# Kernel optimization log

Measured on AMD Instinct MI355X. Metric: run time of the kernel, lower is better.

## Reference

```python
import jax, jax.numpy as jnp
import numpy as np

B, S, H, A = 64, 4096, 256, 128


def entmax15(z):
    # exact entmax-1.5 along the last axis (Peters & Martins 2019)
    z = z / 2.0
    z = z - jnp.max(z, axis=-1, keepdims=True)
    zs = -jnp.sort(-z, axis=-1)                      # descending sort
    n = zs.shape[-1]
    k = jnp.arange(1, n + 1, dtype=z.dtype)
    mean = jnp.cumsum(zs, axis=-1) / k
    mean_sq = jnp.cumsum(zs * zs, axis=-1) / k
    ss = k * (mean_sq - mean * mean)
    delta = jnp.clip((1.0 - ss) / k, 0.0)
    tau = mean - jnp.sqrt(delta)
    k_star = jnp.sum(tau <= zs, axis=-1)             # support size per row
    tau_star = jnp.take_along_axis(tau, (k_star - 1)[..., None], axis=-1)
    return jnp.square(jnp.clip(z - tau_star, 0.0))


def setup_inputs() -> dict:
    key = jax.random.key(0)
    k0, k1, k2, k3, k4 = jax.random.split(key, 5)
    lim1 = 1.0 / np.sqrt(H)
    lim2 = 1.0 / np.sqrt(A)
    return {
        "lstm_output": jax.random.normal(k0, (B, S, H), dtype=jnp.float32),
        "W1": jax.random.uniform(k1, (H, A), jnp.float32, -lim1, lim1),
        "b1": jax.random.uniform(k2, (A,), jnp.float32, -lim1, lim1),
        "W2": jax.random.uniform(k3, (A, 1), jnp.float32, -lim2, lim2),
        "b2": jax.random.uniform(k4, (1,), jnp.float32, -lim2, lim2),
    }


def reference(lstm_output, W1, b1, W2, b2):
    # score MLP: Linear -> Tanh -> Linear -> squeeze(-1)  => [B, S]
    h = jnp.tanh(jnp.einsum("bsh,ha->bsa", lstm_output, W1) + b1)
    scores = (jnp.einsum("bsa,ao->bso", h, W2) + b2)[..., 0]
    weights = entmax15(scores)                       # entmax over seq axis (dim=1)
    context = jnp.einsum("bsh,bs->bh", lstm_output, weights)
    return (context, weights)
```

## Files before the change

### kernel.cpp

```cpp
#include <hip/hip_runtime.h>
#include <hip/hip_bf16.h>

#define BB 64
#define SS 4096
#define HH 256
#define AA 128
#define MT 128
#define WST 264

typedef __fp16 fp16v2 __attribute__((ext_vector_type(2)));
typedef _Float16 half8v __attribute__((ext_vector_type(8)));
typedef float floatx16 __attribute__((ext_vector_type(16)));

__device__ __forceinline__ float fast_tanh(float x) {
    float xc = fminf(fmaxf(x, -9.0f), 9.0f);
    float e = __expf(2.0f * xc);
    return 1.0f - __fdividef(2.0f, e + 1.0f);
}

__global__ void convert_w1(const float* __restrict__ W1, _Float16* __restrict__ Wt) {
    int n = blockIdx.x;
    int k = threadIdx.x;
    Wt[n * HH + k] = (_Float16)W1[k * AA + n];
}

__global__ __launch_bounds__(256, 2) void score_mfma(
    const float* __restrict__ X,
    const _Float16* __restrict__ Wt,
    const float* __restrict__ b1,
    const float* __restrict__ W2,
    const float* __restrict__ b2,
    float* __restrict__ scores)
{
    __shared__ _Float16 Ws2[128 * WST];

    const int tid   = threadIdx.x;
    const int m0    = blockIdx.x * MT;
    const int wid   = tid >> 6;
    const int lane  = tid & 63;
    const int lrow  = lane & 31;
    const int lhalf = lane >> 5;

    #pragma unroll
    for (int p = 0; p < 16; ++p) {
        int idx = tid + p * 256;
        int row = idx >> 5, u = idx & 31;
        *(uint4*)(Ws2 + row * WST + u * 8) =
            *(const uint4*)(Wt + (size_t)row * HH + u * 8);
    }
    __syncthreads();

    floatx16 acc[4];
    #pragma unroll
    for (int nb = 0; nb < 4; ++nb)
        #pragma unroll
        for (int r = 0; r < 16; ++r) acc[nb][r] = 0.0f;

    const float* xrow = X + (size_t)(m0 + wid * 32 + lrow) * HH + lhalf * 8;

    float4 a0 = *(const float4*)(xrow);
    float4 a1 = *(const float4*)(xrow + 4);
    #pragma unroll
    for (int s = 0; s < 16; ++s) {
        float4 n0 = a0, n1 = a1;
        if (s < 15) {
            n0 = *(const float4*)(xrow + (s + 1) * 16);
            n1 = *(const float4*)(xrow + (s + 1) * 16 + 4);
        }
        union { fp16v2 h2[4]; half8v h8; } ua;
        ua.h2[0] = __builtin_amdgcn_cvt_pkrtz(a0.x, a0.y);
        ua.h2[1] = __builtin_amdgcn_cvt_pkrtz(a0.z, a0.w);
        ua.h2[2] = __builtin_amdgcn_cvt_pkrtz(a1.x, a1.y);
        ua.h2[3] = __builtin_amdgcn_cvt_pkrtz(a1.z, a1.w);
        #pragma unroll
        for (int nb = 0; nb < 4; ++nb) {
            half8v bf = *(half8v*)(Ws2 + (nb * 32 + lrow) * WST + s * 16 + lhalf * 8);
            acc[nb] = __builtin_amdgcn_mfma_f32_32x32x16_f16(ua.h8, bf, acc[nb], 0, 0, 0);
        }
        a0 = n0; a1 = n1;
    }

    const float b2v = b2[0];
    float b1v[4], w2v[4];
    #pragma unroll
    for (int nb = 0; nb < 4; ++nb) {
        b1v[nb] = b1[nb * 32 + lrow];
        w2v[nb] = W2[nb * 32 + lrow];
    }
    #pragma unroll
    for (int r = 0; r < 16; ++r) {
        float s = 0.0f;
        #pragma unroll
        for (int nb = 0; nb < 4; ++nb)
            s += fast_tanh(acc[nb][r] + b1v[nb]) * w2v[nb];
        #pragma unroll
        for (int o = 1; o < 32; o <<= 1) s += __shfl_xor(s, o);
        if (lrow == 0) {
            int ridx = (r & 3) + 8 * (r >> 2) + 4 * lhalf;
            scores[m0 + wid * 32 + ridx] = s + b2v;
        }
    }
}

__global__ __launch_bounds__(256) void entmax_ctx_kernel(
    const float* __restrict__ X, float* __restrict__ buf, float* __restrict__ ctx)
{
    __shared__ float sred[8];
    __shared__ int   cnt;
    __shared__ int   sidx[SS];
    __shared__ float swt[SS];

    const int b = blockIdx.x, tid = threadIdx.x;
    const int wid = tid >> 6;
    float* p = buf + (size_t)b * SS;
    const float4* p4 = (const float4*)p;

    if (tid == 0) cnt = 0;

    float z[16];
    #pragma unroll
    for (int jj = 0; jj < 4; ++jj) {
        float4 v = p4[tid * 4 + jj];
        z[jj * 4 + 0] = v.x * 0.5f; z[jj * 4 + 1] = v.y * 0.5f;
        z[jj * 4 + 2] = v.z * 0.5f; z[jj * 4 + 3] = v.w * 0.5f;
    }

    float m = -1e30f;
    #pragma unroll
    for (int j = 0; j < 16; ++j) m = fmaxf(m, z[j]);
    #pragma unroll
    for (int o = 1; o < 64; o <<= 1) m = fmaxf(m, __shfl_xor(m, o));
    if ((tid & 63) == 0) sred[wid] = m;
    __syncthreads();
    m = fmaxf(fmaxf(sred[0], sred[1]), fmaxf(sred[2], sred[3]));
    __syncthreads();
    #pragma unroll
    for (int j = 0; j < 16; ++j) z[j] -= m;

    float lo = -1.0f, hi = 0.0f;
    #pragma unroll 1
    for (int it = 0; it < 10; ++it) {
        float tau = 0.5f * (lo + hi);
        float s0 = 0.f, s1 = 0.f, s2 = 0.f, s3 = 0.f;
        #pragma unroll
        for (int j = 0; j < 16; j += 4) {
            float d0 = fmaxf(z[j]     - tau, 0.0f);
            float d1 = fmaxf(z[j + 1] - tau, 0.0f);
            float d2 = fmaxf(z[j + 2] - tau, 0.0f);
            float d3 = fmaxf(z[j + 3] - tau, 0.0f);
            s0 = fmaf(d0, d0, s0); s1 = fmaf(d1, d1, s1);
            s2 = fmaf(d2, d2, s2); s3 = fmaf(d3, d3, s3);
        }
        float s = (s0 + s1) + (s2 + s3);
        #pragma unroll
        for (int o = 1; o < 64; o <<= 1) s += __shfl_xor(s, o);
        if ((tid & 63) == 0) sred[wid] = s;
        __syncthreads();
        s = (sred[0] + sred[1]) + (sred[2] + sred[3]);
        __syncthreads();
        if (s >= 1.0f) lo = tau; else hi = tau;
    }

    float tau = lo;
    #pragma unroll 1
    for (int it = 0; it < 4; ++it) {
        float s0 = 0.f, s1 = 0.f, t0 = 0.f, t1 = 0.f;
        #pragma unroll
        for (int j = 0; j < 16; j += 2) {
            float d0 = fmaxf(z[j]     - tau, 0.0f);
            float d1 = fmaxf(z[j + 1] - tau, 0.0f);
            s0 = fmaf(d0, d0, s0); s1 = fmaf(d1, d1, s1);
            t0 += d0; t1 += d1;
        }
        float s = s0 + s1, t = t0 + t1;
        #pragma unroll
        for (int o = 1; o < 64; o <<= 1) {
            s += __shfl_xor(s, o);
            t += __shfl_xor(t, o);
        }
        if ((tid & 63) == 0) { sred[wid * 2] = s; sred[wid * 2 + 1] = t; }
        __syncthreads();
        s = (sred[0] + sred[2]) + (sred[4] + sred[6]);
        t = (sred[1] + sred[3]) + (sred[5] + sred[7]);
        __syncthreads();
        tau = fminf(tau + (s - 1.0f) / (2.0f * t + 1e-30f), hi);
    }

    float4* p4w = (float4*)p;
    #pragma unroll
    for (int jj = 0; jj < 4; ++jj) {
        float w[4];
        #pragma unroll
        for (int k = 0; k < 4; ++k) {
            float d = fmaxf(z[jj * 4 + k] - tau, 0.0f);
            w[k] = d * d;
            if (w[k] > 0.0f) {
                int pos = atomicAdd(&cnt, 1);
                sidx[pos] = tid * 16 + jj * 4 + k;
                swt[pos]  = w[k];
            }
        }
        p4w[tid * 4 + jj] = make_float4(w[0], w[1], w[2], w[3]);
    }
    __syncthreads();

    const int n = cnt;
    const float* xb = X + (size_t)b * SS * HH + tid;
    float a0 = 0.f, a1 = 0.f, a2 = 0.f, a3 = 0.f;
    int i = 0;
    for (; i + 4 <= n; i += 4) {
        a0 = fmaf(swt[i    ], xb[(size_t)sidx[i    ] * HH], a0);
        a1 = fmaf(swt[i + 1], xb[(size_t)sidx[i + 1] * HH], a1);
        a2 = fmaf(swt[i + 2], xb[(size_t)sidx[i + 2] * HH], a2);
        a3 = fmaf(swt[i + 3], xb[(size_t)sidx[i + 3] * HH], a3);
    }
    for (; i < n; ++i) a0 = fmaf(swt[i], xb[(size_t)sidx[i] * HH], a0);
    ctx[b * HH + tid] = (a0 + a1) + (a2 + a3);
}

extern "C" void kernel_launch(void* const* d_in, const int* in_sizes, int n_in,
                              void* d_out, int out_size, void* d_ws, size_t ws_size,
                              hipStream_t stream) {
    const float* X  = (const float*)d_in[0];
    const float* W1 = (const float*)d_in[1];
    const float* b1 = (const float*)d_in[2];
    const float* W2 = (const float*)d_in[3];
    const float* b2 = (const float*)d_in[4];

    float* out = (float*)d_out;
    float* ctx = out;
    float* wts = out + BB * HH;
    _Float16* Wt = (_Float16*)d_ws;

    convert_w1<<<AA, HH, 0, stream>>>(W1, Wt);
    score_mfma<<<(BB * SS) / MT, 256, 0, stream>>>(X, Wt, b1, W2, b2, wts);
    entmax_ctx_kernel<<<BB, 256, 0, stream>>>(X, wts, ctx);
}
```

Before: 406.7 us.

## Stage X and W1 tiles through LDS with direct global-to-LDS loads

The score kernel now loops over K in chunks of 64. Each chunk loads both the fp32 X tile and the fp16 W1 tile into XOR-swizzled shared memory using global_load_lds, where before X was read per lane directly from global memory and all of W1 was preloaded. This gives coalesced X loads and cuts LDS per block, so occupancy goes up (launch bounds 3). In exchange it adds two barriers per chunk and gives up the register prefetch overlap between loads and MFMA.

```diff
diff --git a/kernel.cpp b/kernel.cpp
--- a/kernel.cpp
+++ b/kernel.cpp
@@ -6,7 +6,7 @@
 #define HH 256
 #define AA 128
 #define MT 128
-#define WST 264
+#define BK 64
 
 typedef __fp16 fp16v2 __attribute__((ext_vector_type(2)));
 typedef _Float16 half8v __attribute__((ext_vector_type(8)));
@@ -24,7 +24,7 @@
     Wt[n * HH + k] = (_Float16)W1[k * AA + n];
 }
 
-__global__ __launch_bounds__(256, 2) void score_mfma(
+__global__ __launch_bounds__(256, 3) void score_mfma(
     const float* __restrict__ X,
     const _Float16* __restrict__ Wt,
     const float* __restrict__ b1,
@@ -32,7 +32,9 @@
     const float* __restrict__ b2,
     float* __restrict__ scores)
 {
-    __shared__ _Float16 Ws2[128 * WST];
+    __shared__ __align__(16) char smem[49152];
+    float*    Xs = (float*)smem;
+    _Float16* Ws = (_Float16*)(smem + 32768);
 
     const int tid   = threadIdx.x;
     const int m0    = blockIdx.x * MT;
@@ -41,43 +43,59 @@
     const int lrow  = lane & 31;
     const int lhalf = lane >> 5;
 
-    #pragma unroll
-    for (int p = 0; p < 16; ++p) {
-        int idx = tid + p * 256;
-        int row = idx >> 5, u = idx & 31;
-        *(uint4*)(Ws2 + row * WST + u * 8) =
-            *(const uint4*)(Wt + (size_t)row * HH + u * 8);
-    }
-    __syncthreads();
-
     floatx16 acc[4];
     #pragma unroll
     for (int nb = 0; nb < 4; ++nb)
         #pragma unroll
         for (int r = 0; r < 16; ++r) acc[nb][r] = 0.0f;
 
-    const float* xrow = X + (size_t)(m0 + wid * 32 + lrow) * HH + lhalf * 8;
-
-    float4 a0 = *(const float4*)(xrow);
-    float4 a1 = *(const float4*)(xrow + 4);
-    #pragma unroll
-    for (int s = 0; s < 16; ++s) {
-        float4 n0 = a0, n1 = a1;
-        if (s < 15) {
-            n0 = *(const float4*)(xrow + (s + 1) * 16);
-            n1 = *(const float4*)(xrow + (s + 1) * 16 + 4);
-        }
-        union { fp16v2 h2[4]; half8v h8; } ua;
-        ua.h2[0] = __builtin_amdgcn_cvt_pkrtz(a0.x, a0.y);
-        ua.h2[1] = __builtin_amdgcn_cvt_pkrtz(a0.z, a0.w);
-        ua.h2[2] = __builtin_amdgcn_cvt_pkrtz(a1.x, a1.y);
-        ua.h2[3] = __builtin_amdgcn_cvt_pkrtz(a1.z, a1.w);
-        #pragma unroll
-        for (int nb = 0; nb < 4; ++nb) {
-            half8v bf = *(half8v*)(Ws2 + (nb * 32 + lrow) * WST + s * 16 + lhalf * 8);
-            acc[nb] = __builtin_amdgcn_mfma_f32_32x32x16_f16(ua.h8, bf, acc[nb], 0, 0, 0);
-        }
-        a0 = n0; a1 = n1;
+    const int rl  = wid * 32 + lrow;
+    const int swz = rl & 7;
+
+    for (int k0 = 0; k0 < HH; k0 += BK) {
+        #pragma unroll
+        for (int p = 0; p < 8; ++p) {
+            int S = (p * 4 + wid) * 64 + lane;
+            int r = S >> 4;
+            int c = (S & 15) ^ (r & 7);
+            const float* gp = X + (size_t)(m0 + r) * HH + k0 + c * 4;
+            __builtin_amdgcn_global_load_lds(
+                (const __attribute__((address_space(1))) void*)gp,
+                (__attribute__((address_space(3))) void*)(smem + (p * 4 + wid) * 1024),
+                16, 0, 0);
+        }
+        #pragma unroll
+        for (int p = 0; p < 4; ++p) {
+            int S = (p * 4 + wid) * 64 + lane;
+            int r = S >> 3;
+            int c = (S & 7) ^ (r & 7);
+            const _Float16* gp = Wt + (size_t)r * HH + k0 + c * 8;
+            __builtin_amdgcn_global_load_lds(
+                (const __attribute__((address_space(1))) void*)gp,
+                (__attribute__((address_space(3))) void*)(smem + 32768 + (p * 4 + wid) * 1024),
+                16, 0, 0);
+        }
+        __syncthreads();
+
+        #pragma unroll
+        for (int s = 0; s < 4; ++s) {
+            int c0 = s * 4 + lhalf * 2;
+            float4 xa = *(float4*)(Xs + (size_t)(rl * 16 + ((c0    ) ^ swz)) * 4);
+            float4 xb = *(float4*)(Xs + (size_t)(rl * 16 + ((c0 + 1) ^ swz)) * 4);
+            union { fp16v2 h2[4]; half8v h8; } ua;
+            ua.h2[0] = __builtin_amdgcn_cvt_pkrtz(xa.x, xa.y);
+            ua.h2[1] = __builtin_amdgcn_cvt_pkrtz(xa.z, xa.w);
+            ua.h2[2] = __builtin_amdgcn_cvt_pkrtz(xb.x, xb.y);
+            ua.h2[3] = __builtin_amdgcn_cvt_pkrtz(xb.z, xb.w);
+            #pragma unroll
+            for (int nb = 0; nb < 4; ++nb) {
+                int rb = nb * 32 + lrow;
+                int cb = (s * 2 + lhalf) ^ (rb & 7);
+                half8v bf = *(half8v*)(Ws + (size_t)(rb * 8 + cb) * 8);
+                acc[nb] = __builtin_amdgcn_mfma_f32_32x32x16_f16(ua.h8, bf, acc[nb], 0, 0, 0);
+            }
+        }
+        __syncthreads();
     }
 
     const float b2v = b2[0];
```

New measurement: 390.8 us. 1.04x faster.
